# Performance work log

Measured on AMD Instinct MI355X. Metric: run time of the kernel, lower is better.

The kernel has to match this reference:

```python
import jax, jax.numpy as jnp
import numpy as np

N, HID, H, D = 2048, 1024, 16, 64


def setup_inputs() -> dict:
    key = jax.random.key(0)
    ks = jax.random.split(key, 10)
    s_in = 1.0 / np.sqrt(HID)      # Linear(hidden -> H*D) init scale
    s_o = 1.0 / np.sqrt(H * D)     # Linear(H*D -> D) init scale
    return {
        "x": jax.random.normal(ks[0], (N, HID), jnp.float32),
        "history": jnp.zeros((H, N, N), jnp.float32),
        "Wq_w": jax.random.uniform(ks[1], (H * D, HID), jnp.float32, -s_in, s_in),
        "Wq_b": jax.random.uniform(ks[2], (H * D,), jnp.float32, -s_in, s_in),
        "Wk_w": jax.random.uniform(ks[3], (H * D, HID), jnp.float32, -s_in, s_in),
        "Wk_b": jax.random.uniform(ks[4], (H * D,), jnp.float32, -s_in, s_in),
        "Wv_w": jax.random.uniform(ks[5], (H * D, HID), jnp.float32, -s_in, s_in),
        "Wv_b": jax.random.uniform(ks[6], (H * D,), jnp.float32, -s_in, s_in),
        "Wo_w": jax.random.uniform(ks[7], (D, H * D), jnp.float32, -s_o, s_o),
        "Wo_b": jax.random.uniform(ks[8], (D,), jnp.float32, -s_o, s_o),
        "beta": jnp.float32(0.1),
    }


def reference(x, history, Wq_w, Wq_b, Wk_w, Wk_b, Wv_w, Wv_b, Wo_w, Wo_b, beta):
    n = x.shape[0]
    # QKV projections: [N, H*D] -> [H, N, D]
    q = (x @ Wq_w.T + Wq_b).reshape(n, H, D).transpose(1, 0, 2)
    k = (x @ Wk_w.T + Wk_b).reshape(n, H, D).transpose(1, 0, 2)
    v = (x @ Wv_w.T + Wv_b).reshape(n, H, D).transpose(1, 0, 2)
    scores = jnp.einsum('hnd,hmd->hnm', q, k) / np.sqrt(D).astype(np.float32)
    scores = scores + beta * history  # learned additive history bias
    attn = jax.nn.softmax(scores, axis=-1)  # [H, N, N]
    new_history = history + jax.lax.stop_gradient(attn)  # stateful accumulation (detached)
    out = jnp.einsum('hnm,hmd->hnd', attn, v)  # [H, N, D]
    out = out.transpose(1, 0, 2).reshape(n, H * D)
    out = out @ Wo_w.T + Wo_b  # [N, D]
    # dropout is identity (p=0.0 / eval)
    return (out, attn, new_history)
```

## Files before the change

kernel.cpp:

```cpp
#include <hip/hip_runtime.h>
#include <hip/hip_bf16.h>

#define N_TOK 2048
#define HIDDEN 1024
#define NHEAD 16
#define DHEAD 64

typedef __attribute__((ext_vector_type(8))) short bf16x8;
typedef __attribute__((ext_vector_type(4))) float f32x4;

#define WAITV(N) do { asm volatile("s_waitcnt vmcnt(" #N ")" ::: "memory"); \
                      __builtin_amdgcn_sched_barrier(0); } while (0)

__device__ inline unsigned short f2bf(float x) {
    __hip_bfloat16 h = __float2bfloat16(x);
    return *reinterpret_cast<unsigned short*>(&h);
}

__device__ inline f32x4 zero4() {
    f32x4 z;
    z[0] = 0.f; z[1] = 0.f; z[2] = 0.f; z[3] = 0.f;
    return z;
}

__device__ inline void gl_lds16(const unsigned short* g, unsigned short* l) {
    __builtin_amdgcn_global_load_lds(
        (const __attribute__((address_space(1))) unsigned int*)g,
        (__attribute__((address_space(3))) unsigned int*)l, 16, 0, 0);
}

__global__ void cvt4_kernel(const float* __restrict__ x, const float* __restrict__ wq,
                            const float* __restrict__ wk, const float* __restrict__ wv,
                            unsigned short* __restrict__ dst) {
    int i = blockIdx.x * blockDim.x + threadIdx.x;
    const float* src;
    int off;
    if (i < 524288)       { src = x;  off = i; }
    else if (i < 786432)  { src = wq; off = i - 524288; }
    else if (i < 1048576) { src = wk; off = i - 786432; }
    else                  { src = wv; off = i - 1048576; }
    float4 v = reinterpret_cast<const float4*>(src)[off];
    ushort4 o;
    o.x = f2bf(v.x); o.y = f2bf(v.y); o.z = f2bf(v.z); o.w = f2bf(v.w);
    reinterpret_cast<ushort4*>(dst)[i] = o;
}

__launch_bounds__(256)
__global__ void gemm_qkv(const unsigned short* __restrict__ xb,
                         const unsigned short* __restrict__ wb,
                         const float* __restrict__ bq, const float* __restrict__ bk,
                         const float* __restrict__ bv,
                         unsigned short* __restrict__ qb, unsigned short* __restrict__ kb,
                         unsigned short* __restrict__ vt) {
    __shared__ unsigned short As[2][128 * 64];
    __shared__ unsigned short Bs[2][128 * 64];
    const int tid = threadIdx.x;
    const int lane = tid & 63;
    const int w = tid >> 6;
    const int wr = w >> 1, wc = w & 1;
    const int rb = blockIdx.y * 128;
    const int cb = blockIdx.x * 128;
    const int r0 = tid >> 3, c0 = tid & 7;

    f32x4 acc[4][4];
    for (int i = 0; i < 4; i++)
        for (int j = 0; j < 4; j++) acc[i][j] = zero4();

    uint4 va[4], vb4[4];
#pragma unroll
    for (int i = 0; i < 4; i++) {
        va[i]  = *reinterpret_cast<const uint4*>(xb + (size_t)(rb + r0 + 32 * i) * HIDDEN + c0 * 8);
        vb4[i] = *reinterpret_cast<const uint4*>(wb + (size_t)(cb + r0 + 32 * i) * HIDDEN + c0 * 8);
    }
#pragma unroll
    for (int i = 0; i < 4; i++) {
        int row = r0 + 32 * i;
        *reinterpret_cast<uint4*>(As[0] + row * 64 + ((c0 ^ (row & 7)) << 3)) = va[i];
        *reinterpret_cast<uint4*>(Bs[0] + row * 64 + ((c0 ^ (row & 7)) << 3)) = vb4[i];
    }
    __syncthreads();
    int cur = 0;

    for (int kt = 0; kt < 16; ++kt) {
        if (kt < 15) {
#pragma unroll
            for (int i = 0; i < 4; i++) {
                va[i]  = *reinterpret_cast<const uint4*>(xb + (size_t)(rb + r0 + 32 * i) * HIDDEN + (kt + 1) * 64 + c0 * 8);
                vb4[i] = *reinterpret_cast<const uint4*>(wb + (size_t)(cb + r0 + 32 * i) * HIDDEN + (kt + 1) * 64 + c0 * 8);
            }
        }
#pragma unroll
        for (int kk = 0; kk < 2; kk++) {
            bf16x8 a[4], b[4];
#pragma unroll
            for (int mi = 0; mi < 4; mi++) {
                int row = wr * 64 + mi * 16 + (lane & 15);
                a[mi] = *reinterpret_cast<const bf16x8*>(As[cur] + row * 64 + (((kk * 4 + (lane >> 4)) ^ (row & 7)) << 3));
            }
#pragma unroll
            for (int ni = 0; ni < 4; ni++) {
                int row = wc * 64 + ni * 16 + (lane & 15);
                b[ni] = *reinterpret_cast<const bf16x8*>(Bs[cur] + row * 64 + (((kk * 4 + (lane >> 4)) ^ (row & 7)) << 3));
            }
#pragma unroll
            for (int mi = 0; mi < 4; mi++)
#pragma unroll
                for (int ni = 0; ni < 4; ni++)
                    acc[mi][ni] = __builtin_amdgcn_mfma_f32_16x16x32_bf16(a[mi], b[ni], acc[mi][ni], 0, 0, 0);
        }
        if (kt < 15) {
#pragma unroll
            for (int i = 0; i < 4; i++) {
                int row = r0 + 32 * i;
                *reinterpret_cast<uint4*>(As[cur ^ 1] + row * 64 + ((c0 ^ (row & 7)) << 3)) = va[i];
                *reinterpret_cast<uint4*>(Bs[cur ^ 1] + row * 64 + ((c0 ^ (row & 7)) << 3)) = vb4[i];
            }
        }
        __syncthreads();
        cur ^= 1;
    }

    const int region = blockIdx.x >> 3;
    const float* bias = region == 0 ? bq : (region == 1 ? bk : bv);
    unsigned short* dst = region == 0 ? qb : kb;
#pragma unroll
    for (int mi = 0; mi < 4; mi++) {
#pragma unroll
        for (int ni = 0; ni < 4; ni++) {
            int colg = cb + wc * 64 + ni * 16 + (lane & 15);
            int jj = colg & 1023;
            int hh = jj >> 6, d = jj & 63;
            float bval = bias[jj];
#pragma unroll
            for (int r = 0; r < 4; r++) {
                int n = rb + wr * 64 + mi * 16 + ((lane >> 4) << 2) + r;
                unsigned short val = f2bf(acc[mi][ni][r] + bval);
                if (region < 2)
                    dst[((size_t)hh * N_TOK + n) * 64 + d] = val;
                else
                    vt[(((size_t)(hh * 64 + (n >> 5)) * 64 + d) * 32) + (n & 31)] = val;
            }
        }
    }
}

__launch_bounds__(64, 2)
__global__ void attn_fused(const unsigned short* __restrict__ qb,
                           const unsigned short* __restrict__ kb,
                           const unsigned short* __restrict__ vt,
                           const float* __restrict__ hist,
                           const float* __restrict__ beta_p,
                           float* __restrict__ attn_out,
                           float* __restrict__ nh_out,
                           float* __restrict__ hv) {
    __shared__ unsigned short Kbuf[2][2048];
    __shared__ unsigned short Vbuf[2][2048];
    __shared__ unsigned short Psw[512];
    const int lane = threadIdx.x;
    const int g = lane >> 4, q15 = lane & 15;
    const int bid = blockIdx.x;
    const int orig = (bid & 7) * 256 + (bid >> 3);
    const int h = orig >> 7, rb = orig & 127;
    const float beta = beta_p[0];
    const float scale = 0.125f;

    const unsigned short* qsrc = qb + ((size_t)h * N_TOK + rb * 16 + q15) * 64;
    bf16x8 aq0 = *reinterpret_cast<const bf16x8*>(qsrc + 8 * g);
    bf16x8 aq1 = *reinterpret_cast<const bf16x8*>(qsrc + 8 * g + 32);

    const int koff = (lane >> 3) * 64 + (((lane & 7) ^ (lane >> 3)) << 3);
    const int voff = (lane >> 2) * 32 + (((lane & 3) ^ ((lane >> 3) & 3)) << 3);
    const unsigned short* kt0 = kb + (size_t)h * N_TOK * 64;
    const unsigned short* vt0 = vt + (size_t)h * N_TOK * 64;

#define STAGE_K(T, B) do { const unsigned short* _s = kt0 + (size_t)(T) * 2048 + koff; \
        gl_lds16(_s,        &Kbuf[B][0]);    gl_lds16(_s + 512,  &Kbuf[B][512]);   \
        gl_lds16(_s + 1024, &Kbuf[B][1024]); gl_lds16(_s + 1536, &Kbuf[B][1536]); } while (0)
#define STAGE_V(T, B) do { const unsigned short* _s = vt0 + (size_t)(T) * 2048 + voff; \
        gl_lds16(_s,        &Vbuf[B][0]);    gl_lds16(_s + 512,  &Vbuf[B][512]);   \
        gl_lds16(_s + 1024, &Vbuf[B][1024]); gl_lds16(_s + 1536, &Vbuf[B][1536]); } while (0)

    const size_t rowbase = ((size_t)h * N_TOK + rb * 16 + q15) * N_TOK;
    const float* hbase = hist + rowbase + 4 * g;
    float* abase = attn_out + rowbase + 4 * g;
    float* nbase = nh_out + rowbase + 4 * g;

    float m = -1e30f, l = 0.0f;
    f32x4 h4[2], h4n[2];

    STAGE_K(0, 0);
    h4[0] = *reinterpret_cast<const f32x4*>(hbase);
    h4[1] = *reinterpret_cast<const f32x4*>(hbase + 16);

    for (int t = 0; t < 64; ++t) {
        const int cur = t & 1;
        if (t < 63) {
            STAGE_K(t + 1, cur ^ 1);
            h4n[0] = *reinterpret_cast<const f32x4*>(hbase + (t + 1) * 32);
            h4n[1] = *reinterpret_cast<const f32x4*>(hbase + (t + 1) * 32 + 16);
            WAITV(6);
        } else {
            WAITV(0);
        }
        f32x4 s_acc[2];
#pragma unroll
        for (int nt = 0; nt < 2; ++nt) {
            int krow = nt * 16 + q15;
            bf16x8 kf0 = *reinterpret_cast<const bf16x8*>(Kbuf[cur] + krow * 64 + ((g ^ (q15 & 7)) << 3));
            bf16x8 kf1 = *reinterpret_cast<const bf16x8*>(Kbuf[cur] + krow * 64 + (((4 + g) ^ (q15 & 7)) << 3));
            s_acc[nt] = __builtin_amdgcn_mfma_f32_16x16x32_bf16(kf0, aq0, zero4(), 0, 0, 0);
            s_acc[nt] = __builtin_amdgcn_mfma_f32_16x16x32_bf16(kf1, aq1, s_acc[nt], 0, 0, 0);
        }
        float sc[2][4];
#pragma unroll
        for (int nt = 0; nt < 2; ++nt)
#pragma unroll
            for (int r = 0; r < 4; ++r)
                sc[nt][r] = s_acc[nt][r] * scale + beta * h4[nt][r];

        float tm = sc[0][0];
#pragma unroll
        for (int nt = 0; nt < 2; ++nt)
#pragma unroll
            for (int r = 0; r < 4; ++r) tm = fmaxf(tm, sc[nt][r]);
        tm = fmaxf(tm, __shfl_xor(tm, 16));
        tm = fmaxf(tm, __shfl_xor(tm, 32));
        float mn = fmaxf(m, tm);
        float ps = 0.0f;
#pragma unroll
        for (int nt = 0; nt < 2; ++nt)
#pragma unroll
            for (int r = 0; r < 4; ++r) ps += __expf(sc[nt][r] - mn);
        ps += __shfl_xor(ps, 16);
        ps += __shfl_xor(ps, 32);
        l = l * __expf(m - mn) + ps;
        m = mn;

        h4[0] = h4n[0]; h4[1] = h4n[1];
    }
    const float inv_l = 1.0f / l;

    f32x4 oacc[4];
#pragma unroll
    for (int di = 0; di < 4; ++di) oacc[di] = zero4();

    STAGE_V(63, 1);
    h4[0] = *reinterpret_cast<const f32x4*>(hbase + 63 * 32);
    h4[1] = *reinterpret_cast<const f32x4*>(hbase + 63 * 32 + 16);

    f32x4 sa0, sa1, sn0, sn1;

    for (int tt = 0; tt < 64; ++tt) {
        const int t = 63 - tt;
        const int cur = t & 1;
        if (tt > 0) {
            __builtin_nontemporal_store(sa0, reinterpret_cast<f32x4*>(abase + (t + 1) * 32));
            __builtin_nontemporal_store(sa1, reinterpret_cast<f32x4*>(abase + (t + 1) * 32 + 16));
            __builtin_nontemporal_store(sn0, reinterpret_cast<f32x4*>(nbase + (t + 1) * 32));
            __builtin_nontemporal_store(sn1, reinterpret_cast<f32x4*>(nbase + (t + 1) * 32 + 16));
        }
        if (tt < 63) {
            STAGE_K(t - 1, cur ^ 1);
            STAGE_V(t - 1, cur ^ 1);
            h4n[0] = *reinterpret_cast<const f32x4*>(hbase + (t - 1) * 32);
            h4n[1] = *reinterpret_cast<const f32x4*>(hbase + (t - 1) * 32 + 16);
        }
        if (tt == 0)      { WAITV(10); }
        else if (tt < 63) { WAITV(14); }
        else              { WAITV(4);  }

        f32x4 s_acc[2];
#pragma unroll
        for (int nt = 0; nt < 2; ++nt) {
            int krow = nt * 16 + q15;
            bf16x8 kf0 = *reinterpret_cast<const bf16x8*>(Kbuf[cur] + krow * 64 + ((g ^ (q15 & 7)) << 3));
            bf16x8 kf1 = *reinterpret_cast<const bf16x8*>(Kbuf[cur] + krow * 64 + (((4 + g) ^ (q15 & 7)) << 3));
            s_acc[nt] = __builtin_amdgcn_mfma_f32_16x16x32_bf16(kf0, aq0, zero4(), 0, 0, 0);
            s_acc[nt] = __builtin_amdgcn_mfma_f32_16x16x32_bf16(kf1, aq1, s_acc[nt], 0, 0, 0);
        }

#pragma unroll
        for (int nt = 0; nt < 2; ++nt) {
            float a0 = __expf(s_acc[nt][0] * scale + beta * h4[nt][0] - m) * inv_l;
            float a1 = __expf(s_acc[nt][1] * scale + beta * h4[nt][1] - m) * inv_l;
            float a2 = __expf(s_acc[nt][2] * scale + beta * h4[nt][2] - m) * inv_l;
            float a3 = __expf(s_acc[nt][3] * scale + beta * h4[nt][3] - m) * inv_l;
            f32x4 av, nv;
            av[0] = a0; av[1] = a1; av[2] = a2; av[3] = a3;
            nv[0] = a0 + h4[nt][0]; nv[1] = a1 + h4[nt][1];
            nv[2] = a2 + h4[nt][2]; nv[3] = a3 + h4[nt][3];
            if (nt == 0) { sa0 = av; sn0 = nv; } else { sa1 = av; sn1 = nv; }
            ushort4 p;
            p.x = f2bf(a0); p.y = f2bf(a1); p.z = f2bf(a2); p.w = f2bf(a3);
            *reinterpret_cast<ushort4*>(Psw + q15 * 32 + (((4 * nt + g) ^ (q15 & 6)) << 2)) = p;
        }

        {
            bf16x8 pa = *reinterpret_cast<const bf16x8*>(Psw + q15 * 32 + (((2 * g) ^ (q15 & 6)) << 2));
#pragma unroll
            for (int di = 0; di < 4; ++di) {
                int vrow = di * 16 + q15;
                bf16x8 vf = *reinterpret_cast<const bf16x8*>(Vbuf[cur] + vrow * 32 + ((g ^ ((q15 >> 1) & 3)) << 3));
                oacc[di] = __builtin_amdgcn_mfma_f32_16x16x32_bf16(pa, vf, oacc[di], 0, 0, 0);
            }
        }

        h4[0] = h4n[0]; h4[1] = h4n[1];
    }
    __builtin_nontemporal_store(sa0, reinterpret_cast<f32x4*>(abase));
    __builtin_nontemporal_store(sa1, reinterpret_cast<f32x4*>(abase + 16));
    __builtin_nontemporal_store(sn0, reinterpret_cast<f32x4*>(nbase));
    __builtin_nontemporal_store(sn1, reinterpret_cast<f32x4*>(nbase + 16));

#pragma unroll
    for (int di = 0; di < 4; ++di) {
#pragma unroll
        for (int r = 0; r < 4; ++r) {
            int rl = g * 4 + r;
            int d = di * 16 + q15;
            hv[((size_t)h * N_TOK + rb * 16 + rl) * 64 + d] = oacc[di][r];
        }
    }
#undef STAGE_K
#undef STAGE_V
}

__launch_bounds__(256)
__global__ void out_proj(const float* __restrict__ hv, const float* __restrict__ Wo,
                         const float* __restrict__ bo, float* __restrict__ out) {
    __shared__ float wos[64][129];
    const int tid = threadIdx.x;
    const int dd = tid & 63;
    const int w = tid >> 6;
    const int n0 = blockIdx.x * 16;
    float acc[4] = {0.f, 0.f, 0.f, 0.f};
    for (int kc = 0; kc < 1024; kc += 128) {
        __syncthreads();
#pragma unroll
        for (int i = 0; i < 32; i++) {
            int e = tid + 256 * i;
            int r = e >> 7, j = e & 127;
            wos[r][j] = Wo[(size_t)r * 1024 + kc + j];
        }
        __syncthreads();
#pragma unroll 4
        for (int k = 0; k < 128; k++) {
            float wv = wos[dd][k];
            int jg = kc + k;
            const float* hb = hv + ((size_t)(jg >> 6) * N_TOK) * 64 + (jg & 63);
#pragma unroll
            for (int q = 0; q < 4; q++) {
                acc[q] += hb[(size_t)(n0 + w + 4 * q) * 64] * wv;
            }
        }
    }
#pragma unroll
    for (int q = 0; q < 4; q++)
        out[(size_t)(n0 + w + 4 * q) * 64 + dd] = acc[q] + bo[dd];
}

extern "C" void kernel_launch(void* const* d_in, const int* in_sizes, int n_in,
                              void* d_out, int out_size, void* d_ws, size_t ws_size,
                              hipStream_t stream) {
    const float* x    = (const float*)d_in[0];
    const float* hist = (const float*)d_in[1];
    const float* Wq_w = (const float*)d_in[2];
    const float* Wq_b = (const float*)d_in[3];
    const float* Wk_w = (const float*)d_in[4];
    const float* Wk_b = (const float*)d_in[5];
    const float* Wv_w = (const float*)d_in[6];
    const float* Wv_b = (const float*)d_in[7];
    const float* Wo_w = (const float*)d_in[8];
    const float* Wo_b = (const float*)d_in[9];
    const float* beta = (const float*)d_in[10];

    float* out = (float*)d_out;
    float* attn_out = out + 131072;
    float* nh_out = attn_out + (size_t)NHEAD * N_TOK * N_TOK;

    unsigned short* xb  = (unsigned short*)d_ws;
    unsigned short* wb  = xb + (size_t)N_TOK * HIDDEN;
    unsigned short* qb  = wb + (size_t)3 * HIDDEN * HIDDEN;
    unsigned short* kb  = qb + (size_t)N_TOK * HIDDEN;
    unsigned short* vt  = kb + (size_t)N_TOK * HIDDEN;
    float* hvb = (float*)(vt + (size_t)N_TOK * HIDDEN);

    cvt4_kernel<<<5120, 256, 0, stream>>>(x, Wq_w, Wk_w, Wv_w, xb);
    gemm_qkv<<<dim3(24, 16), 256, 0, stream>>>(xb, wb, Wq_b, Wk_b, Wv_b, qb, kb, vt);
    attn_fused<<<2048, 64, 0, stream>>>(qb, kb, vt, hist, beta, attn_out, nh_out, hvb);
    out_proj<<<128, 256, 0, stream>>>(hvb, Wo_w, Wo_b, out);
}
```

Before: 520.7 us.

## Deepen history prefetch to two tiles and delay attn stores in both passes

The history tiles are now prefetched two iterations ahead in a ping-pong register buffer instead of one, and the loops are unrolled by two with branch-free clamped staging so the vmcnt waits are uniform. In the second pass the attention and new-history stores are deferred by two iterations, so the global loads have more time in flight and the loops avoid register copies and conditionals. The cost is more live registers, which may lower occupancy, plus some redundant clamped loads at the loop tails.

Result: no change. 520.5 us (-0.0%).

```diff
diff --git a/kernel.cpp b/kernel.cpp
--- a/kernel.cpp
+++ b/kernel.cpp
@@ -186,22 +186,20 @@
     float* nbase = nh_out + rowbase + 4 * g;
 
     float m = -1e30f, l = 0.0f;
-    f32x4 h4[2], h4n[2];
+    f32x4 h4[2][2];
 
     STAGE_K(0, 0);
-    h4[0] = *reinterpret_cast<const f32x4*>(hbase);
-    h4[1] = *reinterpret_cast<const f32x4*>(hbase + 16);
-
+    h4[0][0] = *reinterpret_cast<const f32x4*>(hbase);
+    h4[0][1] = *reinterpret_cast<const f32x4*>(hbase + 16);
+    h4[1][0] = *reinterpret_cast<const f32x4*>(hbase + 32);
+    h4[1][1] = *reinterpret_cast<const f32x4*>(hbase + 48);
+
+#pragma unroll 2
     for (int t = 0; t < 64; ++t) {
         const int cur = t & 1;
-        if (t < 63) {
-            STAGE_K(t + 1, cur ^ 1);
-            h4n[0] = *reinterpret_cast<const f32x4*>(hbase + (t + 1) * 32);
-            h4n[1] = *reinterpret_cast<const f32x4*>(hbase + (t + 1) * 32 + 16);
-            WAITV(6);
-        } else {
-            WAITV(0);
-        }
+        const int tn = (t < 63) ? (t + 1) : 63;
+        STAGE_K(tn, tn & 1);
+        WAITV(6);
         f32x4 s_acc[2];
 #pragma unroll
         for (int nt = 0; nt < 2; ++nt) {
@@ -216,7 +214,13 @@
         for (int nt = 0; nt < 2; ++nt)
 #pragma unroll
             for (int r = 0; r < 4; ++r)
-                sc[nt][r] = s_acc[nt][r] * scale + beta * h4[nt][r];
+                sc[nt][r] = s_acc[nt][r] * scale + beta * h4[cur][nt][r];
+
+        {
+            const int hp = (t < 62) ? (t + 2) : 63;
+            h4[cur][0] = *reinterpret_cast<const f32x4*>(hbase + hp * 32);
+            h4[cur][1] = *reinterpret_cast<const f32x4*>(hbase + hp * 32 + 16);
+        }
 
         float tm = sc[0][0];
 #pragma unroll
@@ -235,8 +239,6 @@
         ps += __shfl_xor(ps, 32);
         l = l * __expf(m - mn) + ps;
         m = mn;
-
-        h4[0] = h4n[0]; h4[1] = h4n[1];
     }
     const float inv_l = 1.0f / l;
 
@@ -244,73 +246,80 @@
 #pragma unroll
     for (int di = 0; di < 4; ++di) oacc[di] = zero4();
 
+    f32x4 sA[2][2], sN[2][2];
+
+#define P2_BODY(T, CUR, P, HP) do { \
+        f32x4 s_acc[2]; \
+        _Pragma("unroll") \
+        for (int nt = 0; nt < 2; ++nt) { \
+            int krow = nt * 16 + q15; \
+            bf16x8 kf0 = *reinterpret_cast<const bf16x8*>(Kbuf[CUR] + krow * 64 + ((g ^ (q15 & 7)) << 3)); \
+            bf16x8 kf1 = *reinterpret_cast<const bf16x8*>(Kbuf[CUR] + krow * 64 + (((4 + g) ^ (q15 & 7)) << 3)); \
+            s_acc[nt] = __builtin_amdgcn_mfma_f32_16x16x32_bf16(kf0, aq0, zero4(), 0, 0, 0); \
+            s_acc[nt] = __builtin_amdgcn_mfma_f32_16x16x32_bf16(kf1, aq1, s_acc[nt], 0, 0, 0); \
+        } \
+        _Pragma("unroll") \
+        for (int nt = 0; nt < 2; ++nt) { \
+            float a0 = __expf(s_acc[nt][0] * scale + beta * h4[P][nt][0] - m) * inv_l; \
+            float a1 = __expf(s_acc[nt][1] * scale + beta * h4[P][nt][1] - m) * inv_l; \
+            float a2 = __expf(s_acc[nt][2] * scale + beta * h4[P][nt][2] - m) * inv_l; \
+            float a3 = __expf(s_acc[nt][3] * scale + beta * h4[P][nt][3] - m) * inv_l; \
+            f32x4 av, nv; \
+            av[0] = a0; av[1] = a1; av[2] = a2; av[3] = a3; \
+            nv[0] = a0 + h4[P][nt][0]; nv[1] = a1 + h4[P][nt][1]; \
+            nv[2] = a2 + h4[P][nt][2]; nv[3] = a3 + h4[P][nt][3]; \
+            sA[P][nt] = av; sN[P][nt] = nv; \
+            ushort4 p; \
+            p.x = f2bf(a0); p.y = f2bf(a1); p.z = f2bf(a2); p.w = f2bf(a3); \
+            *reinterpret_cast<ushort4*>(Psw + q15 * 32 + (((4 * nt + g) ^ (q15 & 6)) << 2)) = p; \
+        } \
+        h4[P][0] = *reinterpret_cast<const f32x4*>(hbase + (HP) * 32); \
+        h4[P][1] = *reinterpret_cast<const f32x4*>(hbase + (HP) * 32 + 16); \
+        { \
+            bf16x8 pa = *reinterpret_cast<const bf16x8*>(Psw + q15 * 32 + (((2 * g) ^ (q15 & 6)) << 2)); \
+            _Pragma("unroll") \
+            for (int di = 0; di < 4; ++di) { \
+                int vrow = di * 16 + q15; \
+                bf16x8 vf = *reinterpret_cast<const bf16x8*>(Vbuf[CUR] + vrow * 32 + ((g ^ ((q15 >> 1) & 3)) << 3)); \
+                oacc[di] = __builtin_amdgcn_mfma_f32_16x16x32_bf16(pa, vf, oacc[di], 0, 0, 0); \
+            } \
+        } \
+    } while (0)
+
+#define P2_STORE(P, T) do { \
+        __builtin_nontemporal_store(sA[P][0], reinterpret_cast<f32x4*>(abase + (T) * 32)); \
+        __builtin_nontemporal_store(sA[P][1], reinterpret_cast<f32x4*>(abase + (T) * 32 + 16)); \
+        __builtin_nontemporal_store(sN[P][0], reinterpret_cast<f32x4*>(nbase + (T) * 32)); \
+        __builtin_nontemporal_store(sN[P][1], reinterpret_cast<f32x4*>(nbase + (T) * 32 + 16)); \
+    } while (0)
+
     STAGE_V(63, 1);
-    h4[0] = *reinterpret_cast<const f32x4*>(hbase + 63 * 32);
-    h4[1] = *reinterpret_cast<const f32x4*>(hbase + 63 * 32 + 16);
-
-    f32x4 sa0, sa1, sn0, sn1;
-
-    for (int tt = 0; tt < 64; ++tt) {
+    h4[0][0] = *reinterpret_cast<const f32x4*>(hbase + 63 * 32);
+    h4[0][1] = *reinterpret_cast<const f32x4*>(hbase + 63 * 32 + 16);
+    h4[1][0] = *reinterpret_cast<const f32x4*>(hbase + 62 * 32);
+    h4[1][1] = *reinterpret_cast<const f32x4*>(hbase + 62 * 32 + 16);
+
+    STAGE_K(62, 0); STAGE_V(62, 0);
+    WAITV(10);
+    P2_BODY(63, 1, 0, 61);
+    STAGE_K(61, 1); STAGE_V(61, 1);
+    WAITV(10);
+    P2_BODY(62, 0, 1, 60);
+
+#pragma unroll 2
+    for (int tt = 2; tt < 64; ++tt) {
         const int t = 63 - tt;
+        const int p = tt & 1;
         const int cur = t & 1;
-        if (tt > 0) {
-            __builtin_nontemporal_store(sa0, reinterpret_cast<f32x4*>(abase + (t + 1) * 32));
-            __builtin_nontemporal_store(sa1, reinterpret_cast<f32x4*>(abase + (t + 1) * 32 + 16));
-            __builtin_nontemporal_store(sn0, reinterpret_cast<f32x4*>(nbase + (t + 1) * 32));
-            __builtin_nontemporal_store(sn1, reinterpret_cast<f32x4*>(nbase + (t + 1) * 32 + 16));
-        }
-        if (tt < 63) {
-            STAGE_K(t - 1, cur ^ 1);
-            STAGE_V(t - 1, cur ^ 1);
-            h4n[0] = *reinterpret_cast<const f32x4*>(hbase + (t - 1) * 32);
-            h4n[1] = *reinterpret_cast<const f32x4*>(hbase + (t - 1) * 32 + 16);
-        }
-        if (tt == 0)      { WAITV(10); }
-        else if (tt < 63) { WAITV(14); }
-        else              { WAITV(4);  }
-
-        f32x4 s_acc[2];
-#pragma unroll
-        for (int nt = 0; nt < 2; ++nt) {
-            int krow = nt * 16 + q15;
-            bf16x8 kf0 = *reinterpret_cast<const bf16x8*>(Kbuf[cur] + krow * 64 + ((g ^ (q15 & 7)) << 3));
-            bf16x8 kf1 = *reinterpret_cast<const bf16x8*>(Kbuf[cur] + krow * 64 + (((4 + g) ^ (q15 & 7)) << 3));
-            s_acc[nt] = __builtin_amdgcn_mfma_f32_16x16x32_bf16(kf0, aq0, zero4(), 0, 0, 0);
-            s_acc[nt] = __builtin_amdgcn_mfma_f32_16x16x32_bf16(kf1, aq1, s_acc[nt], 0, 0, 0);
-        }
-
-#pragma unroll
-        for (int nt = 0; nt < 2; ++nt) {
-            float a0 = __expf(s_acc[nt][0] * scale + beta * h4[nt][0] - m) * inv_l;
-            float a1 = __expf(s_acc[nt][1] * scale + beta * h4[nt][1] - m) * inv_l;
-            float a2 = __expf(s_acc[nt][2] * scale + beta * h4[nt][2] - m) * inv_l;
-            float a3 = __expf(s_acc[nt][3] * scale + beta * h4[nt][3] - m) * inv_l;
-            f32x4 av, nv;
-            av[0] = a0; av[1] = a1; av[2] = a2; av[3] = a3;
-            nv[0] = a0 + h4[nt][0]; nv[1] = a1 + h4[nt][1];
-            nv[2] = a2 + h4[nt][2]; nv[3] = a3 + h4[nt][3];
-            if (nt == 0) { sa0 = av; sn0 = nv; } else { sa1 = av; sn1 = nv; }
-            ushort4 p;
-            p.x = f2bf(a0); p.y = f2bf(a1); p.z = f2bf(a2); p.w = f2bf(a3);
-            *reinterpret_cast<ushort4*>(Psw + q15 * 32 + (((4 * nt + g) ^ (q15 & 6)) << 2)) = p;
-        }
-
-        {
-            bf16x8 pa = *reinterpret_cast<const bf16x8*>(Psw + q15 * 32 + (((2 * g) ^ (q15 & 6)) << 2));
-#pragma unroll
-            for (int di = 0; di < 4; ++di) {
-                int vrow = di * 16 + q15;
-                bf16x8 vf = *reinterpret_cast<const bf16x8*>(Vbuf[cur] + vrow * 32 + ((g ^ ((q15 >> 1) & 3)) << 3));
-                oacc[di] = __builtin_amdgcn_mfma_f32_16x16x32_bf16(pa, vf, oacc[di], 0, 0, 0);
-            }
-        }
-
-        h4[0] = h4n[0]; h4[1] = h4n[1];
-    }
-    __builtin_nontemporal_store(sa0, reinterpret_cast<f32x4*>(abase));
-    __builtin_nontemporal_store(sa1, reinterpret_cast<f32x4*>(abase + 16));
-    __builtin_nontemporal_store(sn0, reinterpret_cast<f32x4*>(nbase));
-    __builtin_nontemporal_store(sn1, reinterpret_cast<f32x4*>(nbase + 16));
+        P2_STORE(p, t + 2);
+        const int tn = (t > 1) ? (t - 1) : 0;
+        STAGE_K(tn, tn & 1); STAGE_V(tn, tn & 1);
+        WAITV(14);
+        const int hp = (t >= 2) ? (t - 2) : 0;
+        P2_BODY(t, cur, p, hp);
+    }
+    P2_STORE(0, 1);
+    P2_STORE(1, 0);
 
 #pragma unroll
     for (int di = 0; di < 4; ++di) {
@@ -323,6 +332,8 @@
     }
 #undef STAGE_K
 #undef STAGE_V
+#undef P2_BODY
+#undef P2_STORE
 }
 
 __launch_bounds__(256)
```

## Split attention into column-chunked stats and emit kernels with partial reduction

Applied to the files above, without the earlier changes.

Splits the single fused two-pass attention kernel into a stats kernel and an emit kernel. Each kernel divides a row block's key columns into four chunks, giving 8192 blocks instead of 2048. The stats kernel writes per-chunk max and sum, and the emit kernel merges them before writing attn and new_history. Per-chunk P·V partials are summed by a new reduce kernel. The goal is more parallelism and occupancy on a bandwidth-bound kernel, at the cost of two extra launches, extra partial-output traffic, and a kernel boundary between the two passes over history.

Result: slower. 542.2 us (+4.1%).

```diff
diff --git a/kernel.cpp b/kernel.cpp
--- a/kernel.cpp
+++ b/kernel.cpp
@@ -11,6 +11,8 @@
 
 #define WAITV(N) do { asm volatile("s_waitcnt vmcnt(" #N ")" ::: "memory"); \
                       __builtin_amdgcn_sched_barrier(0); } while (0)
+#define LGKM0() do { asm volatile("s_waitcnt lgkmcnt(0)" ::: "memory"); \
+                     __builtin_amdgcn_sched_barrier(0); } while (0)
 
 __device__ inline unsigned short f2bf(float x) {
     __hip_bfloat16 h = __float2bfloat16(x);
@@ -144,23 +146,21 @@
     }
 }
 
-__launch_bounds__(64, 2)
-__global__ void attn_fused(const unsigned short* __restrict__ qb,
+__launch_bounds__(64, 4)
+__global__ void attn_stats(const unsigned short* __restrict__ qb,
                            const unsigned short* __restrict__ kb,
-                           const unsigned short* __restrict__ vt,
                            const float* __restrict__ hist,
                            const float* __restrict__ beta_p,
-                           float* __restrict__ attn_out,
-                           float* __restrict__ nh_out,
-                           float* __restrict__ hv) {
+                           float* __restrict__ m_part,
+                           float* __restrict__ l_part) {
     __shared__ unsigned short Kbuf[2][2048];
-    __shared__ unsigned short Vbuf[2][2048];
-    __shared__ unsigned short Psw[512];
     const int lane = threadIdx.x;
     const int g = lane >> 4, q15 = lane & 15;
     const int bid = blockIdx.x;
-    const int orig = (bid & 7) * 256 + (bid >> 3);
-    const int h = orig >> 7, rb = orig & 127;
+    const int orig = (bid & 7) * 1024 + (bid >> 3);
+    const int h = orig >> 9;
+    const int rb = (orig >> 2) & 127;
+    const int chunk = orig & 3;
     const float beta = beta_p[0];
     const float scale = 0.125f;
 
@@ -169,39 +169,31 @@
     bf16x8 aq1 = *reinterpret_cast<const bf16x8*>(qsrc + 8 * g + 32);
 
     const int koff = (lane >> 3) * 64 + (((lane & 7) ^ (lane >> 3)) << 3);
-    const int voff = (lane >> 2) * 32 + (((lane & 3) ^ ((lane >> 3) & 3)) << 3);
     const unsigned short* kt0 = kb + (size_t)h * N_TOK * 64;
-    const unsigned short* vt0 = vt + (size_t)h * N_TOK * 64;
-
-#define STAGE_K(T, B) do { const unsigned short* _s = kt0 + (size_t)(T) * 2048 + koff; \
+
+#define STAGE_K2(CT, B) do { const unsigned short* _s = kt0 + (size_t)(CT) * 2048 + koff; \
         gl_lds16(_s,        &Kbuf[B][0]);    gl_lds16(_s + 512,  &Kbuf[B][512]);   \
         gl_lds16(_s + 1024, &Kbuf[B][1024]); gl_lds16(_s + 1536, &Kbuf[B][1536]); } while (0)
-#define STAGE_V(T, B) do { const unsigned short* _s = vt0 + (size_t)(T) * 2048 + voff; \
-        gl_lds16(_s,        &Vbuf[B][0]);    gl_lds16(_s + 512,  &Vbuf[B][512]);   \
-        gl_lds16(_s + 1024, &Vbuf[B][1024]); gl_lds16(_s + 1536, &Vbuf[B][1536]); } while (0)
 
     const size_t rowbase = ((size_t)h * N_TOK + rb * 16 + q15) * N_TOK;
-    const float* hbase = hist + rowbase + 4 * g;
-    float* abase = attn_out + rowbase + 4 * g;
-    float* nbase = nh_out + rowbase + 4 * g;
+    const float* hbase = hist + rowbase + chunk * 512 + 4 * g;
+    const int ct0 = chunk * 16;
 
     float m = -1e30f, l = 0.0f;
-    f32x4 h4[2], h4n[2];
-
-    STAGE_K(0, 0);
-    h4[0] = *reinterpret_cast<const f32x4*>(hbase);
-    h4[1] = *reinterpret_cast<const f32x4*>(hbase + 16);
-
-    for (int t = 0; t < 64; ++t) {
+    f32x4 h4[2][2];
+
+    STAGE_K2(ct0, 0);
+    h4[0][0] = *reinterpret_cast<const f32x4*>(hbase);
+    h4[0][1] = *reinterpret_cast<const f32x4*>(hbase + 16);
+    h4[1][0] = *reinterpret_cast<const f32x4*>(hbase + 32);
+    h4[1][1] = *reinterpret_cast<const f32x4*>(hbase + 48);
+
+#pragma unroll 2
+    for (int t = 0; t < 16; ++t) {
         const int cur = t & 1;
-        if (t < 63) {
-            STAGE_K(t + 1, cur ^ 1);
-            h4n[0] = *reinterpret_cast<const f32x4*>(hbase + (t + 1) * 32);
-            h4n[1] = *reinterpret_cast<const f32x4*>(hbase + (t + 1) * 32 + 16);
-            WAITV(6);
-        } else {
-            WAITV(0);
-        }
+        const int tn = (t < 15) ? (t + 1) : 15;
+        STAGE_K2(ct0 + tn, tn & 1);
+        WAITV(6);
         f32x4 s_acc[2];
 #pragma unroll
         for (int nt = 0; nt < 2; ++nt) {
@@ -216,7 +208,13 @@
         for (int nt = 0; nt < 2; ++nt)
 #pragma unroll
             for (int r = 0; r < 4; ++r)
-                sc[nt][r] = s_acc[nt][r] * scale + beta * h4[nt][r];
+                sc[nt][r] = s_acc[nt][r] * scale + beta * h4[cur][nt][r];
+
+        {
+            const int hp = (t < 14) ? (t + 2) : 15;
+            h4[cur][0] = *reinterpret_cast<const f32x4*>(hbase + hp * 32);
+            h4[cur][1] = *reinterpret_cast<const f32x4*>(hbase + hp * 32 + 16);
+        }
 
         float tm = sc[0][0];
 #pragma unroll
@@ -235,64 +233,117 @@
         ps += __shfl_xor(ps, 32);
         l = l * __expf(m - mn) + ps;
         m = mn;
-
-        h4[0] = h4n[0]; h4[1] = h4n[1];
-    }
-    const float inv_l = 1.0f / l;
+    }
+
+    if (lane < 16) {
+        const int base = ((h * 128 + rb) * 4 + chunk) * 16;
+        m_part[base + lane] = m;
+        l_part[base + lane] = l;
+    }
+#undef STAGE_K2
+}
+
+__launch_bounds__(64, 4)
+__global__ void attn_emit(const unsigned short* __restrict__ qb,
+                          const unsigned short* __restrict__ kb,
+                          const unsigned short* __restrict__ vt,
+                          const float* __restrict__ hist,
+                          const float* __restrict__ beta_p,
+                          const float* __restrict__ m_part,
+                          const float* __restrict__ l_part,
+                          float* __restrict__ attn_out,
+                          float* __restrict__ nh_out,
+                          float* __restrict__ opart) {
+    __shared__ unsigned short Kb[2048];
+    __shared__ unsigned short Vb[2048];
+    __shared__ unsigned short Psw[512];
+    const int lane = threadIdx.x;
+    const int g = lane >> 4, q15 = lane & 15;
+    const int bid = blockIdx.x;
+    const int orig = (bid & 7) * 1024 + (bid >> 3);
+    const int h = orig >> 9;
+    const int rb = (orig >> 2) & 127;
+    const int chunk = orig & 3;
+    const float beta = beta_p[0];
+    const float scale = 0.125f;
+
+    const unsigned short* qsrc = qb + ((size_t)h * N_TOK + rb * 16 + q15) * 64;
+    bf16x8 aq0 = *reinterpret_cast<const bf16x8*>(qsrc + 8 * g);
+    bf16x8 aq1 = *reinterpret_cast<const bf16x8*>(qsrc + 8 * g + 32);
+
+    float m_row, inv_l;
+    {
+        const int pbase = (h * 128 + rb) * 4 * 16;
+        float m0 = m_part[pbase + 0 * 16 + q15];
+        float m1 = m_part[pbase + 1 * 16 + q15];
+        float m2 = m_part[pbase + 2 * 16 + q15];
+        float m3 = m_part[pbase + 3 * 16 + q15];
+        float mm = fmaxf(fmaxf(m0, m1), fmaxf(m2, m3));
+        float ll = l_part[pbase + 0 * 16 + q15] * __expf(m0 - mm)
+                 + l_part[pbase + 1 * 16 + q15] * __expf(m1 - mm)
+                 + l_part[pbase + 2 * 16 + q15] * __expf(m2 - mm)
+                 + l_part[pbase + 3 * 16 + q15] * __expf(m3 - mm);
+        m_row = mm;
+        inv_l = 1.0f / ll;
+    }
+
+    const int koff = (lane >> 3) * 64 + (((lane & 7) ^ (lane >> 3)) << 3);
+    const int voff = (lane >> 2) * 32 + (((lane & 3) ^ ((lane >> 3) & 3)) << 3);
+    const unsigned short* kt0 = kb + (size_t)h * N_TOK * 64;
+    const unsigned short* vt0 = vt + (size_t)h * N_TOK * 64;
+
+#define STAGE_K1(CT) do { const unsigned short* _s = kt0 + (size_t)(CT) * 2048 + koff; \
+        gl_lds16(_s,        &Kb[0]);    gl_lds16(_s + 512,  &Kb[512]);   \
+        gl_lds16(_s + 1024, &Kb[1024]); gl_lds16(_s + 1536, &Kb[1536]); } while (0)
+#define STAGE_V1(CT) do { const unsigned short* _s = vt0 + (size_t)(CT) * 2048 + voff; \
+        gl_lds16(_s,        &Vb[0]);    gl_lds16(_s + 512,  &Vb[512]);   \
+        gl_lds16(_s + 1024, &Vb[1024]); gl_lds16(_s + 1536, &Vb[1536]); } while (0)
+
+    const size_t rowbase = ((size_t)h * N_TOK + rb * 16 + q15) * N_TOK;
+    const float* hbase = hist + rowbase + chunk * 512 + 4 * g;
+    float* abase = attn_out + rowbase + chunk * 512 + 4 * g;
+    float* nbase = nh_out + rowbase + chunk * 512 + 4 * g;
+    const int ct0 = chunk * 16;
 
     f32x4 oacc[4];
 #pragma unroll
     for (int di = 0; di < 4; ++di) oacc[di] = zero4();
 
-    STAGE_V(63, 1);
-    h4[0] = *reinterpret_cast<const f32x4*>(hbase + 63 * 32);
-    h4[1] = *reinterpret_cast<const f32x4*>(hbase + 63 * 32 + 16);
-
-    f32x4 sa0, sa1, sn0, sn1;
-
-    for (int tt = 0; tt < 64; ++tt) {
-        const int t = 63 - tt;
-        const int cur = t & 1;
-        if (tt > 0) {
-            __builtin_nontemporal_store(sa0, reinterpret_cast<f32x4*>(abase + (t + 1) * 32));
-            __builtin_nontemporal_store(sa1, reinterpret_cast<f32x4*>(abase + (t + 1) * 32 + 16));
-            __builtin_nontemporal_store(sn0, reinterpret_cast<f32x4*>(nbase + (t + 1) * 32));
-            __builtin_nontemporal_store(sn1, reinterpret_cast<f32x4*>(nbase + (t + 1) * 32 + 16));
-        }
-        if (tt < 63) {
-            STAGE_K(t - 1, cur ^ 1);
-            STAGE_V(t - 1, cur ^ 1);
-            h4n[0] = *reinterpret_cast<const f32x4*>(hbase + (t - 1) * 32);
-            h4n[1] = *reinterpret_cast<const f32x4*>(hbase + (t - 1) * 32 + 16);
-        }
-        if (tt == 0)      { WAITV(10); }
-        else if (tt < 63) { WAITV(14); }
-        else              { WAITV(4);  }
+    f32x4 h4[2][2];
+    STAGE_K1(ct0); STAGE_V1(ct0);
+    h4[0][0] = *reinterpret_cast<const f32x4*>(hbase);
+    h4[0][1] = *reinterpret_cast<const f32x4*>(hbase + 16);
+
+#pragma unroll 2
+    for (int t = 0; t < 16; ++t) {
+        const int p = t & 1;
+        if (t == 0) { WAITV(0); } else { WAITV(4); }
 
         f32x4 s_acc[2];
 #pragma unroll
         for (int nt = 0; nt < 2; ++nt) {
             int krow = nt * 16 + q15;
-            bf16x8 kf0 = *reinterpret_cast<const bf16x8*>(Kbuf[cur] + krow * 64 + ((g ^ (q15 & 7)) << 3));
-            bf16x8 kf1 = *reinterpret_cast<const bf16x8*>(Kbuf[cur] + krow * 64 + (((4 + g) ^ (q15 & 7)) << 3));
+            bf16x8 kf0 = *reinterpret_cast<const bf16x8*>(Kb + krow * 64 + ((g ^ (q15 & 7)) << 3));
+            bf16x8 kf1 = *reinterpret_cast<const bf16x8*>(Kb + krow * 64 + (((4 + g) ^ (q15 & 7)) << 3));
             s_acc[nt] = __builtin_amdgcn_mfma_f32_16x16x32_bf16(kf0, aq0, zero4(), 0, 0, 0);
             s_acc[nt] = __builtin_amdgcn_mfma_f32_16x16x32_bf16(kf1, aq1, s_acc[nt], 0, 0, 0);
         }
 
+        f32x4 sA[2], sN[2];
 #pragma unroll
         for (int nt = 0; nt < 2; ++nt) {
-            float a0 = __expf(s_acc[nt][0] * scale + beta * h4[nt][0] - m) * inv_l;
-            float a1 = __expf(s_acc[nt][1] * scale + beta * h4[nt][1] - m) * inv_l;
-            float a2 = __expf(s_acc[nt][2] * scale + beta * h4[nt][2] - m) * inv_l;
-            float a3 = __expf(s_acc[nt][3] * scale + beta * h4[nt][3] - m) * inv_l;
+            float a0 = __expf(s_acc[nt][0] * scale + beta * h4[p][nt][0] - m_row) * inv_l;
+            float a1 = __expf(s_acc[nt][1] * scale + beta * h4[p][nt][1] - m_row) * inv_l;
+            float a2 = __expf(s_acc[nt][2] * scale + beta * h4[p][nt][2] - m_row) * inv_l;
+            float a3 = __expf(s_acc[nt][3] * scale + beta * h4[p][nt][3] - m_row) * inv_l;
             f32x4 av, nv;
             av[0] = a0; av[1] = a1; av[2] = a2; av[3] = a3;
-            nv[0] = a0 + h4[nt][0]; nv[1] = a1 + h4[nt][1];
-            nv[2] = a2 + h4[nt][2]; nv[3] = a3 + h4[nt][3];
-            if (nt == 0) { sa0 = av; sn0 = nv; } else { sa1 = av; sn1 = nv; }
-            ushort4 p;
-            p.x = f2bf(a0); p.y = f2bf(a1); p.z = f2bf(a2); p.w = f2bf(a3);
-            *reinterpret_cast<ushort4*>(Psw + q15 * 32 + (((4 * nt + g) ^ (q15 & 6)) << 2)) = p;
+            nv[0] = a0 + h4[p][nt][0]; nv[1] = a1 + h4[p][nt][1];
+            nv[2] = a2 + h4[p][nt][2]; nv[3] = a3 + h4[p][nt][3];
+            sA[nt] = av; sN[nt] = nv;
+            ushort4 pp;
+            pp.x = f2bf(a0); pp.y = f2bf(a1); pp.z = f2bf(a2); pp.w = f2bf(a3);
+            *reinterpret_cast<ushort4*>(Psw + q15 * 32 + (((4 * nt + g) ^ (q15 & 6)) << 2)) = pp;
         }
 
         {
@@ -300,17 +351,22 @@
 #pragma unroll
             for (int di = 0; di < 4; ++di) {
                 int vrow = di * 16 + q15;
-                bf16x8 vf = *reinterpret_cast<const bf16x8*>(Vbuf[cur] + vrow * 32 + ((g ^ ((q15 >> 1) & 3)) << 3));
+                bf16x8 vf = *reinterpret_cast<const bf16x8*>(Vb + vrow * 32 + ((g ^ ((q15 >> 1) & 3)) << 3));
                 oacc[di] = __builtin_amdgcn_mfma_f32_16x16x32_bf16(pa, vf, oacc[di], 0, 0, 0);
             }
         }
 
-        h4[0] = h4n[0]; h4[1] = h4n[1];
-    }
-    __builtin_nontemporal_store(sa0, reinterpret_cast<f32x4*>(abase));
-    __builtin_nontemporal_store(sa1, reinterpret_cast<f32x4*>(abase + 16));
-    __builtin_nontemporal_store(sn0, reinterpret_cast<f32x4*>(nbase));
-    __builtin_nontemporal_store(sn1, reinterpret_cast<f32x4*>(nbase + 16));
+        LGKM0();
+        if (t < 15) {
+            STAGE_K1(ct0 + t + 1); STAGE_V1(ct0 + t + 1);
+            h4[p ^ 1][0] = *reinterpret_cast<const f32x4*>(hbase + (t + 1) * 32);
+            h4[p ^ 1][1] = *reinterpret_cast<const f32x4*>(hbase + (t + 1) * 32 + 16);
+        }
+        __builtin_nontemporal_store(sA[0], reinterpret_cast<f32x4*>(abase + t * 32));
+        __builtin_nontemporal_store(sA[1], reinterpret_cast<f32x4*>(abase + t * 32 + 16));
+        __builtin_nontemporal_store(sN[0], reinterpret_cast<f32x4*>(nbase + t * 32));
+        __builtin_nontemporal_store(sN[1], reinterpret_cast<f32x4*>(nbase + t * 32 + 16));
+    }
 
 #pragma unroll
     for (int di = 0; di < 4; ++di) {
@@ -318,11 +374,23 @@
         for (int r = 0; r < 4; ++r) {
             int rl = g * 4 + r;
             int d = di * 16 + q15;
-            hv[((size_t)h * N_TOK + rb * 16 + rl) * 64 + d] = oacc[di][r];
-        }
-    }
-#undef STAGE_K
-#undef STAGE_V
+            opart[((size_t)(chunk * NHEAD + h) * N_TOK + rb * 16 + rl) * 64 + d] = oacc[di][r];
+        }
+    }
+#undef STAGE_K1
+#undef STAGE_V1
+}
+
+__global__ void reduce_hv(const float4* __restrict__ op, float4* __restrict__ hv) {
+    size_t i = (size_t)blockIdx.x * blockDim.x + threadIdx.x;
+    const size_t C = (size_t)NHEAD * N_TOK * DHEAD / 4;
+    float4 a = op[i], b = op[i + C], c = op[i + 2 * C], d = op[i + 3 * C];
+    float4 r;
+    r.x = a.x + b.x + c.x + d.x;
+    r.y = a.y + b.y + c.y + d.y;
+    r.z = a.z + b.z + c.z + d.z;
+    r.w = a.w + b.w + c.w + d.w;
+    hv[i] = r;
 }
 
 __launch_bounds__(256)
@@ -383,10 +451,16 @@
     unsigned short* qb  = wb + (size_t)3 * HIDDEN * HIDDEN;
     unsigned short* kb  = qb + (size_t)N_TOK * HIDDEN;
     unsigned short* vt  = kb + (size_t)N_TOK * HIDDEN;
-    float* hvb = (float*)(vt + (size_t)N_TOK * HIDDEN);
+    float* hvb    = (float*)(vt + (size_t)N_TOK * HIDDEN);
+    float* m_part = hvb + (size_t)N_TOK * HIDDEN;
+    float* l_part = m_part + 16 * 128 * 4 * 16;
+    float* opart  = l_part + 16 * 128 * 4 * 16;
 
     cvt4_kernel<<<5120, 256, 0, stream>>>(x, Wq_w, Wk_w, Wv_w, xb);
     gemm_qkv<<<dim3(24, 16), 256, 0, stream>>>(xb, wb, Wq_b, Wk_b, Wv_b, qb, kb, vt);
-    attn_fused<<<2048, 64, 0, stream>>>(qb, kb, vt, hist, beta, attn_out, nh_out, hvb);
+    attn_stats<<<8192, 64, 0, stream>>>(qb, kb, hist, beta, m_part, l_part);
+    attn_emit<<<8192, 64, 0, stream>>>(qb, kb, vt, hist, beta, m_part, l_part,
+                                       attn_out, nh_out, opart);
+    reduce_hv<<<2048, 256, 0, stream>>>((const float4*)opart, (float4*)hvb);
     out_proj<<<128, 256, 0, stream>>>(hvb, Wo_w, Wo_b, out);
 }
```

## Shrink LDS to single K/V buffers and raise attention occupancy

Applied to the files above, without the earlier changes.

The attention kernel merges the double-buffered K and V LDS arrays into one two-slot array, so the second pass keeps a single K and a single V tile instead of two of each. That cuts LDS per block, and the launch bound goes from 2 to 4 blocks per CU. History prefetch registers are dropped: the next tile's history is loaded into the same registers right after its last use. The second pass now waits for LDS reads to finish before issuing the next tile's loads, so it loses intra-block double buffering and relies on more resident waves to hide latency.

Result: no change. 520.0 us (-0.1%).

```diff
diff --git a/kernel.cpp b/kernel.cpp
--- a/kernel.cpp
+++ b/kernel.cpp
@@ -11,6 +11,8 @@
 
 #define WAITV(N) do { asm volatile("s_waitcnt vmcnt(" #N ")" ::: "memory"); \
                       __builtin_amdgcn_sched_barrier(0); } while (0)
+#define LGKM0() do { asm volatile("s_waitcnt lgkmcnt(0)" ::: "memory"); \
+                     __builtin_amdgcn_sched_barrier(0); } while (0)
 
 __device__ inline unsigned short f2bf(float x) {
     __hip_bfloat16 h = __float2bfloat16(x);
@@ -144,7 +146,7 @@
     }
 }
 
-__launch_bounds__(64, 2)
+__launch_bounds__(64, 4)
 __global__ void attn_fused(const unsigned short* __restrict__ qb,
                            const unsigned short* __restrict__ kb,
                            const unsigned short* __restrict__ vt,
@@ -153,8 +155,7 @@
                            float* __restrict__ attn_out,
                            float* __restrict__ nh_out,
                            float* __restrict__ hv) {
-    __shared__ unsigned short Kbuf[2][2048];
-    __shared__ unsigned short Vbuf[2][2048];
+    __shared__ unsigned short KV[2][2048];
     __shared__ unsigned short Psw[512];
     const int lane = threadIdx.x;
     const int g = lane >> 4, q15 = lane & 15;
@@ -174,11 +175,11 @@
     const unsigned short* vt0 = vt + (size_t)h * N_TOK * 64;
 
 #define STAGE_K(T, B) do { const unsigned short* _s = kt0 + (size_t)(T) * 2048 + koff; \
-        gl_lds16(_s,        &Kbuf[B][0]);    gl_lds16(_s + 512,  &Kbuf[B][512]);   \
-        gl_lds16(_s + 1024, &Kbuf[B][1024]); gl_lds16(_s + 1536, &Kbuf[B][1536]); } while (0)
+        gl_lds16(_s,        &KV[B][0]);    gl_lds16(_s + 512,  &KV[B][512]);   \
+        gl_lds16(_s + 1024, &KV[B][1024]); gl_lds16(_s + 1536, &KV[B][1536]); } while (0)
 #define STAGE_V(T, B) do { const unsigned short* _s = vt0 + (size_t)(T) * 2048 + voff; \
-        gl_lds16(_s,        &Vbuf[B][0]);    gl_lds16(_s + 512,  &Vbuf[B][512]);   \
-        gl_lds16(_s + 1024, &Vbuf[B][1024]); gl_lds16(_s + 1536, &Vbuf[B][1536]); } while (0)
+        gl_lds16(_s,        &KV[B][0]);    gl_lds16(_s + 512,  &KV[B][512]);   \
+        gl_lds16(_s + 1024, &KV[B][1024]); gl_lds16(_s + 1536, &KV[B][1536]); } while (0)
 
     const size_t rowbase = ((size_t)h * N_TOK + rb * 16 + q15) * N_TOK;
     const float* hbase = hist + rowbase + 4 * g;
@@ -186,7 +187,7 @@
     float* nbase = nh_out + rowbase + 4 * g;
 
     float m = -1e30f, l = 0.0f;
-    f32x4 h4[2], h4n[2];
+    f32x4 h4[2];
 
     STAGE_K(0, 0);
     h4[0] = *reinterpret_cast<const f32x4*>(hbase);
@@ -196,8 +197,6 @@
         const int cur = t & 1;
         if (t < 63) {
             STAGE_K(t + 1, cur ^ 1);
-            h4n[0] = *reinterpret_cast<const f32x4*>(hbase + (t + 1) * 32);
-            h4n[1] = *reinterpret_cast<const f32x4*>(hbase + (t + 1) * 32 + 16);
             WAITV(6);
         } else {
             WAITV(0);
@@ -206,8 +205,8 @@
 #pragma unroll
         for (int nt = 0; nt < 2; ++nt) {
             int krow = nt * 16 + q15;
-            bf16x8 kf0 = *reinterpret_cast<const bf16x8*>(Kbuf[cur] + krow * 64 + ((g ^ (q15 & 7)) << 3));
-            bf16x8 kf1 = *reinterpret_cast<const bf16x8*>(Kbuf[cur] + krow * 64 + (((4 + g) ^ (q15 & 7)) << 3));
+            bf16x8 kf0 = *reinterpret_cast<const bf16x8*>(KV[cur] + krow * 64 + ((g ^ (q15 & 7)) << 3));
+            bf16x8 kf1 = *reinterpret_cast<const bf16x8*>(KV[cur] + krow * 64 + (((4 + g) ^ (q15 & 7)) << 3));
             s_acc[nt] = __builtin_amdgcn_mfma_f32_16x16x32_bf16(kf0, aq0, zero4(), 0, 0, 0);
             s_acc[nt] = __builtin_amdgcn_mfma_f32_16x16x32_bf16(kf1, aq1, s_acc[nt], 0, 0, 0);
         }
@@ -217,6 +216,11 @@
 #pragma unroll
             for (int r = 0; r < 4; ++r)
                 sc[nt][r] = s_acc[nt][r] * scale + beta * h4[nt][r];
+
+        if (t < 63) {
+            h4[0] = *reinterpret_cast<const f32x4*>(hbase + (t + 1) * 32);
+            h4[1] = *reinterpret_cast<const f32x4*>(hbase + (t + 1) * 32 + 16);
+        }
 
         float tm = sc[0][0];
 #pragma unroll
@@ -235,8 +239,6 @@
         ps += __shfl_xor(ps, 32);
         l = l * __expf(m - mn) + ps;
         m = mn;
-
-        h4[0] = h4n[0]; h4[1] = h4n[1];
     }
     const float inv_l = 1.0f / l;
 
@@ -244,41 +246,26 @@
 #pragma unroll
     for (int di = 0; di < 4; ++di) oacc[di] = zero4();
 
+    STAGE_K(63, 0);
     STAGE_V(63, 1);
     h4[0] = *reinterpret_cast<const f32x4*>(hbase + 63 * 32);
     h4[1] = *reinterpret_cast<const f32x4*>(hbase + 63 * 32 + 16);
 
-    f32x4 sa0, sa1, sn0, sn1;
-
     for (int tt = 0; tt < 64; ++tt) {
         const int t = 63 - tt;
-        const int cur = t & 1;
-        if (tt > 0) {
-            __builtin_nontemporal_store(sa0, reinterpret_cast<f32x4*>(abase + (t + 1) * 32));
-            __builtin_nontemporal_store(sa1, reinterpret_cast<f32x4*>(abase + (t + 1) * 32 + 16));
-            __builtin_nontemporal_store(sn0, reinterpret_cast<f32x4*>(nbase + (t + 1) * 32));
-            __builtin_nontemporal_store(sn1, reinterpret_cast<f32x4*>(nbase + (t + 1) * 32 + 16));
-        }
-        if (tt < 63) {
-            STAGE_K(t - 1, cur ^ 1);
-            STAGE_V(t - 1, cur ^ 1);
-            h4n[0] = *reinterpret_cast<const f32x4*>(hbase + (t - 1) * 32);
-            h4n[1] = *reinterpret_cast<const f32x4*>(hbase + (t - 1) * 32 + 16);
-        }
-        if (tt == 0)      { WAITV(10); }
-        else if (tt < 63) { WAITV(14); }
-        else              { WAITV(4);  }
+        if (tt == 0) { WAITV(0); } else { WAITV(4); }
 
         f32x4 s_acc[2];
 #pragma unroll
         for (int nt = 0; nt < 2; ++nt) {
             int krow = nt * 16 + q15;
-            bf16x8 kf0 = *reinterpret_cast<const bf16x8*>(Kbuf[cur] + krow * 64 + ((g ^ (q15 & 7)) << 3));
-            bf16x8 kf1 = *reinterpret_cast<const bf16x8*>(Kbuf[cur] + krow * 64 + (((4 + g) ^ (q15 & 7)) << 3));
+            bf16x8 kf0 = *reinterpret_cast<const bf16x8*>(KV[0] + krow * 64 + ((g ^ (q15 & 7)) << 3));
+            bf16x8 kf1 = *reinterpret_cast<const bf16x8*>(KV[0] + krow * 64 + (((4 + g) ^ (q15 & 7)) << 3));
             s_acc[nt] = __builtin_amdgcn_mfma_f32_16x16x32_bf16(kf0, aq0, zero4(), 0, 0, 0);
             s_acc[nt] = __builtin_amdgcn_mfma_f32_16x16x32_bf16(kf1, aq1, s_acc[nt], 0, 0, 0);
         }
 
+        f32x4 sA[2], sN[2];
 #pragma unroll
         for (int nt = 0; nt < 2; ++nt) {
             float a0 = __expf(s_acc[nt][0] * scale + beta * h4[nt][0] - m) * inv_l;
@@ -289,10 +276,15 @@
             av[0] = a0; av[1] = a1; av[2] = a2; av[3] = a3;
             nv[0] = a0 + h4[nt][0]; nv[1] = a1 + h4[nt][1];
             nv[2] = a2 + h4[nt][2]; nv[3] = a3 + h4[nt][3];
-            if (nt == 0) { sa0 = av; sn0 = nv; } else { sa1 = av; sn1 = nv; }
-            ushort4 p;
-            p.x = f2bf(a0); p.y = f2bf(a1); p.z = f2bf(a2); p.w = f2bf(a3);
-            *reinterpret_cast<ushort4*>(Psw + q15 * 32 + (((4 * nt + g) ^ (q15 & 6)) << 2)) = p;
+            sA[nt] = av; sN[nt] = nv;
+            ushort4 pp;
+            pp.x = f2bf(a0); pp.y = f2bf(a1); pp.z = f2bf(a2); pp.w = f2bf(a3);
+            *reinterpret_cast<ushort4*>(Psw + q15 * 32 + (((4 * nt + g) ^ (q15 & 6)) << 2)) = pp;
+        }
+
+        if (tt < 63) {
+            h4[0] = *reinterpret_cast<const f32x4*>(hbase + (t - 1) * 32);
+            h4[1] = *reinterpret_cast<const f32x4*>(hbase + (t - 1) * 32 + 16);
         }
 
         {
@@ -300,17 +292,21 @@
 #pragma unroll
             for (int di = 0; di < 4; ++di) {
                 int vrow = di * 16 + q15;
-                bf16x8 vf = *reinterpret_cast<const bf16x8*>(Vbuf[cur] + vrow * 32 + ((g ^ ((q15 >> 1) & 3)) << 3));
+                bf16x8 vf = *reinterpret_cast<const bf16x8*>(KV[1] + vrow * 32 + ((g ^ ((q15 >> 1) & 3)) << 3));
                 oacc[di] = __builtin_amdgcn_mfma_f32_16x16x32_bf16(pa, vf, oacc[di], 0, 0, 0);
             }
         }
 
-        h4[0] = h4n[0]; h4[1] = h4n[1];
-    }
-    __builtin_nontemporal_store(sa0, reinterpret_cast<f32x4*>(abase));
-    __builtin_nontemporal_store(sa1, reinterpret_cast<f32x4*>(abase + 16));
-    __builtin_nontemporal_store(sn0, reinterpret_cast<f32x4*>(nbase));
-    __builtin_nontemporal_store(sn1, reinterpret_cast<f32x4*>(nbase + 16));
+        LGKM0();
+        if (tt < 63) {
+            STAGE_K(t - 1, 0);
+            STAGE_V(t - 1, 1);
+        }
+        __builtin_nontemporal_store(sA[0], reinterpret_cast<f32x4*>(abase + t * 32));
+        __builtin_nontemporal_store(sA[1], reinterpret_cast<f32x4*>(abase + t * 32 + 16));
+        __builtin_nontemporal_store(sN[0], reinterpret_cast<f32x4*>(nbase + t * 32));
+        __builtin_nontemporal_store(sN[1], reinterpret_cast<f32x4*>(nbase + t * 32 + 16));
+    }
 
 #pragma unroll
     for (int di = 0; di < 4; ++di) {
```
